# Performance work log

Measured on AMD Instinct MI355X. Metric: run time of the kernel, lower is better.

## Reference

```python
import jax, jax.numpy as jnp
import numpy as np

N = 100000   # nodes
E = 1600000  # edges
F = 256      # n_feats
H = 128      # n_hidden
HEADS = 8
C = 64       # n_class


def setup_inputs() -> dict:
    key = jax.random.key(0)
    ks = jax.random.split(key, 32)
    rn = lambda k, shape, s=0.05: jax.random.normal(k, shape, jnp.float32) * s
    return {
        'x': rn(ks[0], (N, F), 1.0),
        'src': jax.random.randint(ks[1], (E,), 0, N, jnp.int32),
        'dst': jax.random.randint(ks[2], (E,), 0, N, jnp.int32),
        'in_W': rn(ks[3], (F, H)), 'in_b': jnp.zeros((H,), jnp.float32),
        # layer 0 (concat=True, dim_out = H // HEADS)
        'q0_W': rn(ks[4], (H, H)), 'q0_b': jnp.zeros((H,), jnp.float32),
        'k0_W': rn(ks[5], (H, H)), 'k0_b': jnp.zeros((H,), jnp.float32),
        'v0_W': rn(ks[6], (H, H)), 'v0_b': jnp.zeros((H,), jnp.float32),
        'res0_W': rn(ks[7], (H, H)), 'res0_b': jnp.zeros((H,), jnp.float32),
        'gate0_W': rn(ks[8], (3 * H, 1)),
        'ln0_g': jnp.ones((H,), jnp.float32), 'ln0_b': jnp.zeros((H,), jnp.float32),
        # layer 1 (last: dim_out = C per head, concat=False, only_gate residual)
        'q1_W': rn(ks[9], (H, C * HEADS)), 'q1_b': jnp.zeros((C * HEADS,), jnp.float32),
        'k1_W': rn(ks[10], (H, C * HEADS)), 'k1_b': jnp.zeros((C * HEADS,), jnp.float32),
        'v1_W': rn(ks[11], (H, C * HEADS)), 'v1_b': jnp.zeros((C * HEADS,), jnp.float32),
        'res1_W': rn(ks[12], (H, C)), 'res1_b': jnp.zeros((C,), jnp.float32),
        'gate1_W': rn(ks[13], (3 * C, 1)),
    }


def _attn(x, qW, qb, kW, kb, vW, vb, src, dst, concat):
    n = x.shape[0]
    q = (x @ qW + qb).reshape(n, HEADS, -1)
    k = (x @ kW + kb).reshape(n, HEADS, -1)
    v = (x @ vW + vb).reshape(n, HEADS, -1)
    d = q.shape[-1]
    # u_dot_v: per-edge dot(q[src], k[dst]) -> [E, HEADS]
    s = jnp.einsum('ehd,ehd->eh', q[src], k[dst]) / jnp.sqrt(jnp.float32(d))
    # edge_softmax: segment softmax over incoming edges of each dst node
    m = jax.ops.segment_max(s, dst, num_segments=n)
    e = jnp.exp(s - m[dst])
    z = jax.ops.segment_sum(e, dst, num_segments=n)
    p = e / z[dst]
    # u_mul_e_sum: scatter-add v[src] * p to dst
    out = jax.ops.segment_sum(v[src] * p[:, :, None], dst, num_segments=n)
    return out.reshape(n, -1) if concat else out.mean(axis=1)


def _layernorm(x, g, b, eps=1e-5):
    mu = x.mean(-1, keepdims=True)
    var = ((x - mu) ** 2).mean(-1, keepdims=True)
    return (x - mu) / jnp.sqrt(var + eps) * g + b


def _gated_res(x, res, rW, rb, gW, ln_g=None, ln_b=None, only_gate=False):
    res = res @ rW + rb
    gate = jax.nn.sigmoid(jnp.concatenate([x, res, x - res], axis=-1) @ gW)
    out = x * gate + res * (1.0 - gate)
    if only_gate:
        return out
    return jax.nn.relu(_layernorm(out, ln_g, ln_b))


def reference(x, src, dst, in_W, in_b,
              q0_W, q0_b, k0_W, k0_b, v0_W, v0_b, res0_W, res0_b, gate0_W, ln0_g, ln0_b,
              q1_W, q1_b, k1_W, k1_b, v1_W, v1_b, res1_W, res1_b, gate1_W):
    h = x @ in_W + in_b
    a0 = _attn(h, q0_W, q0_b, k0_W, k0_b, v0_W, v0_b, src, dst, concat=True)
    h = _gated_res(a0, h, res0_W, res0_b, gate0_W, ln0_g, ln0_b, only_gate=False)
    a1 = _attn(h, q1_W, q1_b, k1_W, k1_b, v1_W, v1_b, src, dst, concat=False)
    out = _gated_res(a1, h, res1_W, res1_b, gate1_W, only_gate=True)
    return out
```

## Files before the change

kernel.cpp:

```cpp
#include <hip/hip_runtime.h>


typedef unsigned short u16;
typedef __attribute__((ext_vector_type(8))) unsigned short ushort8;
typedef __attribute__((ext_vector_type(8))) short short8v;
typedef __attribute__((ext_vector_type(4))) float f32x4;
typedef __attribute__((ext_vector_type(2))) float f32x2;

__device__ __forceinline__ float bf2f(unsigned short u) {
    return __uint_as_float(((unsigned)u) << 16);
}
__device__ __forceinline__ unsigned short f2bf(float f) {
    unsigned u = __float_as_uint(f);
    unsigned r = 0x7fffu + ((u >> 16) & 1u);
    return (unsigned short)((u + r) >> 16);
}
__device__ __forceinline__ unsigned char f2fp8(float f) {
    return (unsigned char)__builtin_amdgcn_cvt_pk_fp8_f32(f, 0.f, 0, false);
}

__device__ __forceinline__ void gload16(const void* gp, const void* lp) {
    __builtin_amdgcn_global_load_lds(
        (const __attribute__((address_space(1))) unsigned*)(uintptr_t)gp,
        (__attribute__((address_space(3))) unsigned*)(unsigned)(uintptr_t)lp,
        16, 0, 0);
}

__global__ void prep_k(const float* __restrict__ q1W, const float* __restrict__ k1W,
                       const float* __restrict__ v1W, const float* __restrict__ r1W,
                       u16* __restrict__ arena) {
    int i = blockIdx.x * 256 + threadIdx.x + 98304;
    if (i >= 303104) return;
    float val;
    if (i < 294912) {
        int j = i - 98304;
        int row = j >> 7, kk = j & 127;
        int p = row / 768, rr = row - p * 768;
        int sec = rr >> 8, c = p * 256 + (rr & 255);
        const float* s = (sec == 0) ? q1W : (sec == 1) ? k1W : v1W;
        val = s[kk * 512 + c];
    } else {
        int j = i - 294912;
        int n = j >> 7, kk = j & 127;
        val = r1W[kk * 64 + n];
    }
    arena[i] = f2bf(val);
}

__global__ void cw_k(const float* __restrict__ inW, const float* __restrict__ in_b,
                     const float* __restrict__ q0W, const float* __restrict__ k0W,
                     const float* __restrict__ v0W, const float* __restrict__ r0W,
                     const float* __restrict__ q0b, const float* __restrict__ k0b,
                     const float* __restrict__ v0b, const float* __restrict__ r0b,
                     u16* __restrict__ cwt, float* __restrict__ cwb) {
    int i = blockIdx.x * 256 + threadIdx.x;
    if (i < 131072) {
        int n = i >> 8, k = i & 255;
        int sec = n >> 7, c = n & 127;
        const float* s = (sec == 0) ? q0W : (sec == 1) ? k0W : (sec == 2) ? v0W : r0W;
        float acc = 0.f;
        for (int j = 0; j < 128; ++j) acc = fmaf(inW[k * 128 + j], s[j * 128 + c], acc);
        cwt[(size_t)n * 256 + k] = f2bf(acc);
    } else if (i < 131584) {
        int n = i - 131072;
        int sec = n >> 7, c = n & 127;
        const float* s = (sec == 0) ? q0W : (sec == 1) ? k0W : (sec == 2) ? v0W : r0W;
        const float* b = (sec == 0) ? q0b : (sec == 1) ? k0b : (sec == 2) ? v0b : r0b;
        float acc = b[c];
        for (int j = 0; j < 128; ++j) acc = fmaf(in_b[j], s[j * 128 + c], acc);
        cwb[n] = acc;
    }
}

__global__ void bias_k(const float* __restrict__ q1b, const float* __restrict__ k1b,
                       const float* __restrict__ v1b, const float* __restrict__ r1b,
                       float* __restrict__ out) {
    int i = blockIdx.x * 256 + threadIdx.x;
    if (i >= 1600) return;
    if (i < 1536) {
        int p = i / 768, rr = i - p * 768;
        int sec = rr >> 8, c = p * 256 + (rr & 255);
        out[i] = (sec == 0) ? q1b[c] : (sec == 1) ? k1b[c] : v1b[c];
    } else {
        out[i] = r1b[i - 1536];
    }
}

__global__ void cvt_k(const float* __restrict__ in, u16* __restrict__ out, int n8) {
    int i = blockIdx.x * 256 + threadIdx.x;
    if (i >= n8) return;
    float4 a = *(const float4*)(in + (size_t)i * 8);
    float4 b = *(const float4*)(in + (size_t)i * 8 + 4);
    ushort8 o = {f2bf(a.x), f2bf(a.y), f2bf(a.z), f2bf(a.w),
                 f2bf(b.x), f2bf(b.y), f2bf(b.z), f2bf(b.w)};
    *(ushort8*)(out + (size_t)i * 8) = o;
}

template <int MODE, int K>
__global__ __launch_bounds__(256) void mgemm7(const u16* __restrict__ A,
                                              const u16* __restrict__ Bt,
                                              const float* __restrict__ bias,
                                              void* __restrict__ C,
                                              float* __restrict__ C2,
                                              int M, int MB, int ny, int Nvalid) {
    __shared__ __align__(16) unsigned char smem[36864];
    u16* As = (u16*)smem;
    u16* Bs = (u16*)(smem + 16384);
    int id = blockIdx.x;
    int xcd = id & 7, rest = id >> 3;
    int y = rest % ny;
    int x = (rest / ny) * 8 + xcd;
    if (x >= MB) return;
    const int bm = x * 128;
    const int bn = y * 128;
    const int t = threadIdx.x, lane = t & 63, wid = t >> 6;
    const int wm = (wid >> 1) * 64, wn = (wid & 1) * 64;
    const int jlog = ((lane & 7) ^ (lane >> 3)) * 8;
    f32x4 acc[4][4] = {};
    for (int k0 = 0; k0 < K; k0 += 64) {
#pragma unroll
        for (int c2 = 0; c2 < 4; ++c2) {
            int seg = c2 * 4 + wid;
            int row = seg * 8 + (lane >> 3);
            int ga = bm + row; if (ga >= M) ga = 0;
            gload16(A + (size_t)ga * K + k0 + jlog, (const char*)As + seg * 1024);
            int gb = bn + row; if (gb >= Nvalid) gb = 0;
            gload16(Bt + (size_t)gb * K + k0 + jlog, (const char*)Bs + seg * 1024);
        }
        __syncthreads();
#pragma unroll
        for (int ks = 0; ks < 2; ++ks) {
            const int jx = ks * 4 + (lane >> 4);
            short8v af[4], bfr[4];
#pragma unroll
            for (int i = 0; i < 4; ++i) {
                int ra = wm + i * 16 + (lane & 15);
                af[i] = *(const short8v*)((const char*)As + ra * 128 + ((jx ^ (ra & 7)) << 4));
                int rb = wn + i * 16 + (lane & 15);
                bfr[i] = *(const short8v*)((const char*)Bs + rb * 128 + ((jx ^ (rb & 7)) << 4));
            }
#pragma unroll
            for (int mi = 0; mi < 4; ++mi)
#pragma unroll
                for (int ni = 0; ni < 4; ++ni)
                    acc[mi][ni] = __builtin_amdgcn_mfma_f32_16x16x32_bf16(
                        af[mi], bfr[ni], acc[mi][ni], 0, 0, 0);
        }
        if (k0 + 64 < K) __syncthreads();
    }
    const int sec = y;
    bool fp8lds = false;
    int gsecoff = 0, rowbytes = 0;
    if (MODE == 1) {
        if (sec == 0)      { fp8lds = true; gsecoff = 0;   rowbytes = 512; }
        else if (sec == 2) { fp8lds = true; gsecoff = 384; rowbytes = 512; }
    } else if (MODE >= 2) {
        if (sec < 2)                  { fp8lds = true; gsecoff = sec * 128;             rowbytes = 1024; }
        else if (sec >= 4 && sec < 6) { fp8lds = true; gsecoff = 768 + (sec - 4) * 128; rowbytes = 1024; }
    }
    if (fp8lds) {
        unsigned char* tile = smem;
        __syncthreads();
#pragma unroll
        for (int ni = 0; ni < 4; ++ni) {
            int lcol = wn + ni * 16 + (lane & 15);
            float bs = bias[bn + lcol];
#pragma unroll
            for (int mi = 0; mi < 4; ++mi) {
#pragma unroll
                for (int j = 0; j < 4; ++j) {
                    int lrow = wm + mi * 16 + (lane >> 4) * 4 + j;
                    float val = acc[mi][ni][j] + bs;
                    tile[lrow * 144 + ((((lcol >> 4) ^ (lrow & 7)) << 4) | (lcol & 15))] =
                        f2fp8(val * 16.f);
                }
            }
        }
        __syncthreads();
#pragma unroll
        for (int it = 0; it < 4; ++it) {
            int lin = it * 256 + t;
            int row = lin >> 3, ch = lin & 7;
            int crow = bm + row;
            if (crow < M) {
                const float4 vsrc = *(const float4*)(tile + row * 144 + ((ch ^ (row & 7)) << 4));
                *(float4*)((unsigned char*)C + (size_t)crow * rowbytes + gsecoff + ch * 16) = vsrc;
            }
        }
        return;
    }
    bool bf16lds = false;
    if (MODE == 1 && sec == 1)             { bf16lds = true; gsecoff = 128; rowbytes = 512; }
    else if (MODE >= 2 && sec >= 2 && sec < 4) {
        bf16lds = true; gsecoff = 256 + (sec - 2) * 256; rowbytes = 1024;
    }
    if (bf16lds) {
        unsigned char* tile = smem;
        __syncthreads();
#pragma unroll
        for (int ni = 0; ni < 4; ++ni) {
            int lcol = wn + ni * 16 + (lane & 15);
            float bs = bias[bn + lcol];
            int by = lcol * 2, ch = by >> 4;
#pragma unroll
            for (int mi = 0; mi < 4; ++mi) {
#pragma unroll
                for (int j = 0; j < 4; ++j) {
                    int lrow = wm + mi * 16 + (lane >> 4) * 4 + j;
                    float val = acc[mi][ni][j] + bs;
                    *(u16*)(tile + lrow * 272 + ((ch ^ (lrow & 7)) << 4) + (by & 15)) = f2bf(val);
                }
            }
        }
        __syncthreads();
#pragma unroll
        for (int it = 0; it < 8; ++it) {
            int lin = it * 256 + t;
            int row = lin >> 4, ch = lin & 15;
            int crow = bm + row;
            if (crow < M) {
                const float4 vsrc = *(const float4*)(tile + row * 272 + ((ch ^ (row & 7)) << 4));
                *(float4*)((unsigned char*)C + (size_t)crow * rowbytes + gsecoff + ch * 16) = vsrc;
            }
        }
        return;
    }
#pragma unroll
    for (int ni = 0; ni < 4; ++ni) {
        int lcol = wn + ni * 16 + (lane & 15);
        int ccol = bn + lcol;
        if (ccol >= Nvalid) continue;
        float bs = bias[ccol];
#pragma unroll
        for (int mi = 0; mi < 4; ++mi) {
#pragma unroll
            for (int j = 0; j < 4; ++j) {
                int crow = bm + wm + mi * 16 + (lane >> 4) * 4 + j;
                if (crow >= M) continue;
                float val = acc[mi][ni][j] + bs;
                if (MODE == 1) {
                    C2[(size_t)crow * 128 + lcol] = val;
                } else {
                    C2[(size_t)crow * 64 + lcol] = val;
                }
            }
        }
    }
}

__global__ void zero1_k(int* __restrict__ a, int n) {
    int i = blockIdx.x * 256 + threadIdx.x;
    if (i < n) a[i] = 0;
}

__global__ void hist_k(const int* __restrict__ dst, int* __restrict__ cnt,
                       int* __restrict__ rank, int E) {
    int i = blockIdx.x * 256 + threadIdx.x;
    if (i < E) rank[i] = atomicAdd(&cnt[dst[i]], 1);
}

__global__ void blocksum_k(const int* __restrict__ cnt, int* __restrict__ bsum, int n) {
    __shared__ int sd[256];
    int i = blockIdx.x * 256 + threadIdx.x;
    sd[threadIdx.x] = (i < n) ? cnt[i] : 0;
    __syncthreads();
    for (int off = 128; off > 0; off >>= 1) {
        if (threadIdx.x < off) sd[threadIdx.x] += sd[threadIdx.x + off];
        __syncthreads();
    }
    if (threadIdx.x == 0) bsum[blockIdx.x] = sd[0];
}

__global__ void scanb_k(int* bsum, int nb) {
    __shared__ int tmp[512];
    int t = threadIdx.x;
    tmp[t] = (t < nb) ? bsum[t] : 0;
    __syncthreads();
    for (int off = 1; off < 512; off <<= 1) {
        int v = (t >= off) ? tmp[t - off] : 0;
        __syncthreads();
        tmp[t] += v;
        __syncthreads();
    }
    if (t < nb) bsum[t] = (t ? tmp[t - 1] : 0);
}

__global__ void scanc_k(const int* __restrict__ cnt, const int* __restrict__ bsum,
                        int* __restrict__ row_off, int n, int E) {
    __shared__ int tmp[256];
    int b = blockIdx.x, t = threadIdx.x;
    int i = b * 256 + t;
    int own = (i < n) ? cnt[i] : 0;
    tmp[t] = own;
    __syncthreads();
    for (int off = 1; off < 256; off <<= 1) {
        int v = (t >= off) ? tmp[t - off] : 0;
        __syncthreads();
        tmp[t] += v;
        __syncthreads();
    }
    if (i < n) row_off[i] = bsum[b] + tmp[t] - own;
    if (b == 0 && t == 0) row_off[n] = E;
}

__global__ void scatter_k(const int* __restrict__ src, const int* __restrict__ dst,
                          const int* __restrict__ row_off, const int* __restrict__ rank,
                          int* __restrict__ csr_src, int E) {
    int i = blockIdx.x * 256 + threadIdx.x;
    if (i < E) csr_src[row_off[dst[i]] + rank[i]] = src[i];
}

__global__ __launch_bounds__(256) void attn0_k(const unsigned char* __restrict__ qkv,
                                               const int* __restrict__ row_off,
                                               const int* __restrict__ csr,
                                               const float* __restrict__ res0o,
                                               const float* __restrict__ gw,
                                               const float* __restrict__ lng,
                                               const float* __restrict__ lnb,
                                               u16* __restrict__ h1, int n) {
    int w = (blockIdx.x * 256 + threadIdx.x) >> 6;
    int lane = threadIdx.x & 63;
    if (w >= n) return;
    int beg = row_off[w], end = row_off[w + 1];
    unsigned kv = *(const unsigned*)(qkv + (size_t)w * 512 + 128 + 4 * lane);
    const float KS = (0.25f / 16.f) * 1.44269504f;
    float k0f = bf2f((u16)kv) * KS, k1f = bf2f((u16)(kv >> 16)) * KS;
    float den = 0.f, num0 = 0.f, num1 = 0.f;
    int e = beg;
    for (; e + 4 <= end; e += 4) {
        int s0 = csr[e], s1 = csr[e + 1], s2 = csr[e + 2], s3 = csr[e + 3];
        const unsigned char* r0 = qkv + (size_t)s0 * 512;
        const unsigned char* r1 = qkv + (size_t)s1 * 512;
        const unsigned char* r2 = qkv + (size_t)s2 * 512;
        const unsigned char* r3 = qkv + (size_t)s3 * 512;
        int qa = *(const unsigned short*)(r0 + 2 * lane);
        int qb = *(const unsigned short*)(r1 + 2 * lane);
        int qc = *(const unsigned short*)(r2 + 2 * lane);
        int qd = *(const unsigned short*)(r3 + 2 * lane);
        int va = *(const unsigned short*)(r0 + 384 + 2 * lane);
        int vb = *(const unsigned short*)(r1 + 384 + 2 * lane);
        int vc = *(const unsigned short*)(r2 + 384 + 2 * lane);
        int vd = *(const unsigned short*)(r3 + 384 + 2 * lane);
        f32x2 qaf = __builtin_amdgcn_cvt_pk_f32_fp8(qa, false);
        f32x2 qbf = __builtin_amdgcn_cvt_pk_f32_fp8(qb, false);
        f32x2 qcf = __builtin_amdgcn_cvt_pk_f32_fp8(qc, false);
        f32x2 qdf = __builtin_amdgcn_cvt_pk_f32_fp8(qd, false);
        float pa = qaf.x * k0f + qaf.y * k1f;
        float pb = qbf.x * k0f + qbf.y * k1f;
        float pc = qcf.x * k0f + qcf.y * k1f;
        float pd = qdf.x * k0f + qdf.y * k1f;
#pragma unroll
        for (int off = 1; off < 8; off <<= 1) {
            pa += __shfl_xor(pa, off); pb += __shfl_xor(pb, off);
            pc += __shfl_xor(pc, off); pd += __shfl_xor(pd, off);
        }
        float wa = exp2f(pa), wb = exp2f(pb);
        float wc = exp2f(pc), wd = exp2f(pd);
        den += (wa + wb) + (wc + wd);
        f32x2 vaf = __builtin_amdgcn_cvt_pk_f32_fp8(va, false);
        f32x2 vbf = __builtin_amdgcn_cvt_pk_f32_fp8(vb, false);
        f32x2 vcf = __builtin_amdgcn_cvt_pk_f32_fp8(vc, false);
        f32x2 vdf = __builtin_amdgcn_cvt_pk_f32_fp8(vd, false);
        num0 = fmaf(wa, vaf.x, num0); num1 = fmaf(wa, vaf.y, num1);
        num0 = fmaf(wb, vbf.x, num0); num1 = fmaf(wb, vbf.y, num1);
        num0 = fmaf(wc, vcf.x, num0); num1 = fmaf(wc, vcf.y, num1);
        num0 = fmaf(wd, vdf.x, num0); num1 = fmaf(wd, vdf.y, num1);
    }
    for (; e < end; ++e) {
        int s = csr[e];
        const unsigned char* r = qkv + (size_t)s * 512;
        int qv = *(const unsigned short*)(r + 2 * lane);
        f32x2 qf = __builtin_amdgcn_cvt_pk_f32_fp8(qv, false);
        float p = qf.x * k0f + qf.y * k1f;
        p += __shfl_xor(p, 1);
        p += __shfl_xor(p, 2);
        p += __shfl_xor(p, 4);
        float wt = exp2f(p);
        den += wt;
        int vv = *(const unsigned short*)(r + 384 + 2 * lane);
        f32x2 vf = __builtin_amdgcn_cvt_pk_f32_fp8(vv, false);
        num0 = fmaf(wt, vf.x, num0); num1 = fmaf(wt, vf.y, num1);
    }
    float inv = (end > beg) ? (1.f / den) * (1.f / 16.f) : 0.f;
    float x1 = num0 * inv, x2 = num1 * inv;
    f32x2 rv  = *(const f32x2*)(res0o + (size_t)w * 128 + 2 * lane);
    f32x2 ga  = *(const f32x2*)(gw + 2 * lane);
    f32x2 gb  = *(const f32x2*)(gw + 128 + 2 * lane);
    f32x2 gc  = *(const f32x2*)(gw + 256 + 2 * lane);
    float ca1 = ga.x + gc.x, ca2 = ga.y + gc.y;
    float cr1 = gb.x - gc.x, cr2 = gb.y - gc.y;
    float dot = x1 * ca1 + x2 * ca2 + rv.x * cr1 + rv.y * cr2;
#pragma unroll
    for (int off = 1; off < 64; off <<= 1) dot += __shfl_xor(dot, off);
    float g = 1.f / (1.f + __expf(-dot));
    float o1 = x1 * g + rv.x * (1.f - g);
    float o2 = x2 * g + rv.y * (1.f - g);
    float s = o1 + o2;
#pragma unroll
    for (int off = 1; off < 64; off <<= 1) s += __shfl_xor(s, off);
    float mu = s * (1.f / 128.f);
    float d1 = o1 - mu, d2 = o2 - mu;
    float vs = d1 * d1 + d2 * d2;
#pragma unroll
    for (int off = 1; off < 64; off <<= 1) vs += __shfl_xor(vs, off);
    float rstd = rsqrtf(vs * (1.f / 128.f) + 1e-5f);
    f32x2 lg = *(const f32x2*)(lng + 2 * lane);
    f32x2 lb = *(const f32x2*)(lnb + 2 * lane);
    float y1 = fmaxf(d1 * rstd * lg.x + lb.x, 0.f);
    float y2 = fmaxf(d2 * rstd * lg.y + lb.y, 0.f);
    unsigned pk = (unsigned)f2bf(y1) | ((unsigned)f2bf(y2) << 16);
    ((unsigned*)h1)[(size_t)w * 64 + lane] = pk;
}

__device__ __forceinline__ void attn1_core(const unsigned char* __restrict__ qkv,
                                           const int* __restrict__ csr,
                                           int w, int lane, int beg, int end,
                                           float& o0, float& o1, float& o2, float& o3) {
    const float KS = (0.125f / 16.f) * 1.44269504f;
    float kr0, kr1, kr2, kr3;
    {
        uint2 kk2 = *(const uint2*)(qkv + (size_t)w * 1024 + 256 + 8 * lane);
        kr0 = bf2f((u16)kk2.x) * KS; kr1 = bf2f((u16)(kk2.x >> 16)) * KS;
        kr2 = bf2f((u16)kk2.y) * KS; kr3 = bf2f((u16)(kk2.y >> 16)) * KS;
    }
    float den = 0.f, num0 = 0.f, num1 = 0.f, num2 = 0.f, num3 = 0.f;
    int e = beg;
    for (; e + 4 <= end; e += 4) {
        int s0 = csr[e], s1 = csr[e + 1], s2 = csr[e + 2], s3 = csr[e + 3];
        const unsigned char* r0 = qkv + (size_t)s0 * 1024;
        const unsigned char* r1 = qkv + (size_t)s1 * 1024;
        const unsigned char* r2 = qkv + (size_t)s2 * 1024;
        const unsigned char* r3 = qkv + (size_t)s3 * 1024;
        unsigned qa = *(const unsigned*)(r0 + 4 * lane);
        unsigned qb = *(const unsigned*)(r1 + 4 * lane);
        unsigned qc = *(const unsigned*)(r2 + 4 * lane);
        unsigned qd = *(const unsigned*)(r3 + 4 * lane);
        unsigned va = *(const unsigned*)(r0 + 768 + 4 * lane);
        unsigned vb = *(const unsigned*)(r1 + 768 + 4 * lane);
        unsigned vc = *(const unsigned*)(r2 + 768 + 4 * lane);
        unsigned vd = *(const unsigned*)(r3 + 768 + 4 * lane);
        f32x2 qa0 = __builtin_amdgcn_cvt_pk_f32_fp8((int)qa, false);
        f32x2 qa1 = __builtin_amdgcn_cvt_pk_f32_fp8((int)qa, true);
        f32x2 qb0 = __builtin_amdgcn_cvt_pk_f32_fp8((int)qb, false);
        f32x2 qb1 = __builtin_amdgcn_cvt_pk_f32_fp8((int)qb, true);
        f32x2 qc0 = __builtin_amdgcn_cvt_pk_f32_fp8((int)qc, false);
        f32x2 qc1 = __builtin_amdgcn_cvt_pk_f32_fp8((int)qc, true);
        f32x2 qd0 = __builtin_amdgcn_cvt_pk_f32_fp8((int)qd, false);
        f32x2 qd1 = __builtin_amdgcn_cvt_pk_f32_fp8((int)qd, true);
        float pa = qa0.x * kr0 + qa0.y * kr1 + qa1.x * kr2 + qa1.y * kr3;
        float pb = qb0.x * kr0 + qb0.y * kr1 + qb1.x * kr2 + qb1.y * kr3;
        float pc = qc0.x * kr0 + qc0.y * kr1 + qc1.x * kr2 + qc1.y * kr3;
        float pd = qd0.x * kr0 + qd0.y * kr1 + qd1.x * kr2 + qd1.y * kr3;
#pragma unroll
        for (int off = 1; off < 16; off <<= 1) {
            pa += __shfl_xor(pa, off); pb += __shfl_xor(pb, off);
            pc += __shfl_xor(pc, off); pd += __shfl_xor(pd, off);
        }
        float wa = exp2f(pa), wb = exp2f(pb);
        float wc = exp2f(pc), wd = exp2f(pd);
        den += (wa + wb) + (wc + wd);
        f32x2 va0 = __builtin_amdgcn_cvt_pk_f32_fp8((int)va, false);
        f32x2 va1 = __builtin_amdgcn_cvt_pk_f32_fp8((int)va, true);
        f32x2 vb0 = __builtin_amdgcn_cvt_pk_f32_fp8((int)vb, false);
        f32x2 vb1 = __builtin_amdgcn_cvt_pk_f32_fp8((int)vb, true);
        f32x2 vc0 = __builtin_amdgcn_cvt_pk_f32_fp8((int)vc, false);
        f32x2 vc1 = __builtin_amdgcn_cvt_pk_f32_fp8((int)vc, true);
        f32x2 vd0 = __builtin_amdgcn_cvt_pk_f32_fp8((int)vd, false);
        f32x2 vd1 = __builtin_amdgcn_cvt_pk_f32_fp8((int)vd, true);
        num0 = fmaf(wa, va0.x, num0); num1 = fmaf(wa, va0.y, num1);
        num2 = fmaf(wa, va1.x, num2); num3 = fmaf(wa, va1.y, num3);
        num0 = fmaf(wb, vb0.x, num0); num1 = fmaf(wb, vb0.y, num1);
        num2 = fmaf(wb, vb1.x, num2); num3 = fmaf(wb, vb1.y, num3);
        num0 = fmaf(wc, vc0.x, num0); num1 = fmaf(wc, vc0.y, num1);
        num2 = fmaf(wc, vc1.x, num2); num3 = fmaf(wc, vc1.y, num3);
        num0 = fmaf(wd, vd0.x, num0); num1 = fmaf(wd, vd0.y, num1);
        num2 = fmaf(wd, vd1.x, num2); num3 = fmaf(wd, vd1.y, num3);
    }
    for (; e < end; ++e) {
        int s = csr[e];
        const unsigned char* r = qkv + (size_t)s * 1024;
        unsigned qv = *(const unsigned*)(r + 4 * lane);
        f32x2 q0 = __builtin_amdgcn_cvt_pk_f32_fp8((int)qv, false);
        f32x2 q1 = __builtin_amdgcn_cvt_pk_f32_fp8((int)qv, true);
        float p = q0.x * kr0 + q0.y * kr1 + q1.x * kr2 + q1.y * kr3;
#pragma unroll
        for (int off = 1; off < 16; off <<= 1) p += __shfl_xor(p, off);
        float wt = exp2f(p);
        den += wt;
        unsigned vv = *(const unsigned*)(r + 768 + 4 * lane);
        f32x2 v0 = __builtin_amdgcn_cvt_pk_f32_fp8((int)vv, false);
        f32x2 v1 = __builtin_amdgcn_cvt_pk_f32_fp8((int)vv, true);
        num0 = fmaf(wt, v0.x, num0); num1 = fmaf(wt, v0.y, num1);
        num2 = fmaf(wt, v1.x, num2); num3 = fmaf(wt, v1.y, num3);
    }
    float inv = (end > beg) ? 1.f / den : 0.f;
    o0 = num0 * inv; o1 = num1 * inv; o2 = num2 * inv; o3 = num3 * inv;
    o0 += __shfl_xor(o0, 16); o1 += __shfl_xor(o1, 16);
    o2 += __shfl_xor(o2, 16); o3 += __shfl_xor(o3, 16);
    o0 += __shfl_xor(o0, 32); o1 += __shfl_xor(o1, 32);
    o2 += __shfl_xor(o2, 32); o3 += __shfl_xor(o3, 32);
}

__global__ __launch_bounds__(256) void attn1f_k(const unsigned char* __restrict__ qkv,
                                                const int* __restrict__ row_off,
                                                const int* __restrict__ csr,
                                                float* __restrict__ out, int n) {
    int w = (blockIdx.x * 256 + threadIdx.x) >> 6;
    int lane = threadIdx.x & 63;
    if (w >= n) return;
    int beg = row_off[w], end = row_off[w + 1];
    float o0, o1, o2, o3;
    attn1_core(qkv, csr, w, lane, beg, end, o0, o1, o2, o3);
    if (lane < 16) {
        const float HS = 1.f / 128.f;
        *(float4*)(out + ((size_t)w << 6) + lane * 4) =
            make_float4(o0 * HS, o1 * HS, o2 * HS, o3 * HS);
    }
}

__global__ __launch_bounds__(256) void attn1g_k(const unsigned char* __restrict__ qkv,
                                                const int* __restrict__ row_off,
                                                const int* __restrict__ csr,
                                                const float* __restrict__ a1,
                                                const float* __restrict__ res1o,
                                                const float* __restrict__ gw,
                                                float* __restrict__ out, int n) {
    int w = (blockIdx.x * 256 + threadIdx.x) >> 6;
    int lane = threadIdx.x & 63;
    if (w >= n) return;
    int beg = row_off[w], end = row_off[w + 1];
    float o0, o1, o2, o3;
    attn1_core(qkv, csr, w, lane, beg, end, o0, o1, o2, o3);
    const float HS = 1.f / 128.f;
    int ll = lane & 15;
    size_t base = (size_t)w * 64 + ll * 4;
    float4 ap = *(const float4*)(a1 + base);
    float4 rp = *(const float4*)(res1o + base);
    float4 g0 = *(const float4*)(gw + ll * 4);
    float4 g1 = *(const float4*)(gw + 64 + ll * 4);
    float4 g2 = *(const float4*)(gw + 128 + ll * 4);
    float xv0 = ap.x + o0 * HS, xv1 = ap.y + o1 * HS;
    float xv2 = ap.z + o2 * HS, xv3 = ap.w + o3 * HS;
    float dot = xv0 * (g0.x + g2.x) + xv1 * (g0.y + g2.y)
              + xv2 * (g0.z + g2.z) + xv3 * (g0.w + g2.w)
              + rp.x * (g1.x - g2.x) + rp.y * (g1.y - g2.y)
              + rp.z * (g1.z - g2.z) + rp.w * (g1.w - g2.w);
#pragma unroll
    for (int off = 1; off < 16; off <<= 1) dot += __shfl_xor(dot, off);
    float g = 1.f / (1.f + __expf(-dot));
    if (lane < 16) {
        float4 ov;
        ov.x = xv0 * g + rp.x * (1.f - g);
        ov.y = xv1 * g + rp.y * (1.f - g);
        ov.z = xv2 * g + rp.z * (1.f - g);
        ov.w = xv3 * g + rp.w * (1.f - g);
        *(float4*)(out + base) = ov;
    }
}

extern "C" void kernel_launch(void* const* d_in, const int* in_sizes, int n_in,
                              void* d_out, int out_size, void* d_ws, size_t ws_size,
                              hipStream_t stream) {
    const float* x    = (const float*)d_in[0];
    const int*   src  = (const int*)d_in[1];
    const int*   dst  = (const int*)d_in[2];
    const float* in_W = (const float*)d_in[3];
    const float* in_b = (const float*)d_in[4];
    const float* q0W = (const float*)d_in[5];  const float* q0b = (const float*)d_in[6];
    const float* k0W = (const float*)d_in[7];  const float* k0b = (const float*)d_in[8];
    const float* v0W = (const float*)d_in[9];  const float* v0b = (const float*)d_in[10];
    const float* r0W = (const float*)d_in[11]; const float* r0b = (const float*)d_in[12];
    const float* g0W = (const float*)d_in[13];
    const float* ln0g = (const float*)d_in[14]; const float* ln0b = (const float*)d_in[15];
    const float* q1W = (const float*)d_in[16]; const float* q1b = (const float*)d_in[17];
    const float* k1W = (const float*)d_in[18]; const float* k1b = (const float*)d_in[19];
    const float* v1W = (const float*)d_in[20]; const float* v1b = (const float*)d_in[21];
    const float* r1W = (const float*)d_in[22]; const float* r1b = (const float*)d_in[23];
    const float* g1W = (const float*)d_in[24];

    const int N = in_sizes[0] / 256;
    const int E = in_sizes[1];
    (void)ws_size; (void)n_in; (void)out_size;

    auto rnd = [](size_t b) { return (b + 255) & ~(size_t)255; };
    char* base = (char*)d_ws;
    const size_t S_f = rnd((size_t)N * 128 * 4);
    size_t o = 0;
    int* row_off = (int*)(base + o); o += rnd(((size_t)N + 1) * 4);
    int* csr     = (int*)(base + o); o += rnd((size_t)E * 4);
    u16* warena  = (u16*)(base + o); o += rnd((size_t)(303104 + 131072) * 2);
    float* barena = (float*)(base + o); o += rnd((size_t)(1600 + 512) * 4);
    char* RB = base + o;
    int* cnt  = (int*)RB;
    int* bsum = (int*)(RB + rnd((size_t)N * 4));
    unsigned char* QKV0 = (unsigned char*)RB;
    unsigned char* PASS = (unsigned char*)RB;
    float* res0o = (float*)(RB + S_f);
    u16*   x_bf  = (u16*)(RB + 2 * S_f);
    float* a1    = (float*)(RB + 2 * S_f);
    float* res1o = (float*)(RB + 2 * S_f + rnd((size_t)N * 64 * 4));
    int*   rank  = (int*)(RB + 3 * S_f);
    u16*   h1    = (u16*)(RB + 3 * S_f);

    u16* qkv1t0 = warena + 98304;
    u16* qkv1t1 = warena + 196608;
    u16* cwt    = warena + 303104;
    float* qkv1b = barena;
    float* cwb   = barena + 1600;

    dim3 blk(256);
    int nwb = (N * 64 + 255) / 256;
    int nb  = (N + 255) / 256;
    int mb  = (N + 127) / 128;
    int xch = (mb + 7) / 8;

    prep_k<<<(303104 - 98304 + 255) / 256, blk, 0, stream>>>(q1W, k1W, v1W, r1W, warena);
    cw_k<<<(131584 + 255) / 256, blk, 0, stream>>>(in_W, in_b, q0W, k0W, v0W, r0W,
                                                   q0b, k0b, v0b, r0b, cwt, cwb);
    bias_k<<<7, blk, 0, stream>>>(q1b, k1b, v1b, r1b, barena);
    cvt_k<<<(N * 32 + 255) / 256, blk, 0, stream>>>(x, x_bf, N * 32);

    zero1_k<<<nb, blk, 0, stream>>>(cnt, N);
    hist_k<<<(E + 255) / 256, blk, 0, stream>>>(dst, cnt, rank, E);
    blocksum_k<<<nb, blk, 0, stream>>>(cnt, bsum, N);
    scanb_k<<<1, 512, 0, stream>>>(bsum, nb);
    scanc_k<<<nb, blk, 0, stream>>>(cnt, bsum, row_off, N, E);
    scatter_k<<<(E + 255) / 256, blk, 0, stream>>>(src, dst, row_off, rank, csr, E);

    mgemm7<1, 256><<<8 * 4 * xch, blk, 0, stream>>>(x_bf, cwt, cwb, QKV0, res0o,
                                                    N, mb, 4, 512);
    attn0_k<<<nwb, blk, 0, stream>>>(QKV0, row_off, csr, res0o, g0W, ln0g, ln0b, h1, N);

    mgemm7<2, 128><<<8 * 6 * xch, blk, 0, stream>>>(h1, qkv1t0, qkv1b, PASS,
                                                    nullptr, N, mb, 6, 768);
    attn1f_k<<<nwb, blk, 0, stream>>>(PASS, row_off, csr, a1, N);

    mgemm7<3, 128><<<8 * 7 * xch, blk, 0, stream>>>(h1, qkv1t1, qkv1b + 768, PASS,
                                                    res1o, N, mb, 7, 832);
    attn1g_k<<<nwb, blk, 0, stream>>>(PASS, row_off, csr, a1, res1o, g1W,
                                      (float*)d_out, N);
}
```

Before: 730.7 us.

## Fuse layer-1 split GEMMs and attention passes into one GEMM plus one attention

Layer 1 used to run as two halves, each with its own GEMM and attention pass, with K stored in bf16 and an intermediate a1 buffer. Now a single GEMM produces Q, K and V for all heads in fp8 with a 1536-byte row stride, and writes the residual projection straight into the output buffer. One attention kernel then processes 8 lanes per head group with 8 elements per lane and applies the gate in the same pass. This removes a launch pair, one CSR traversal and the a1/res1o round trips, at the cost of storing K in fp8 (lower precision) and higher register use per lane.

```diff
diff --git a/kernel.cpp b/kernel.cpp
--- a/kernel.cpp
+++ b/kernel.cpp
@@ -29,21 +29,14 @@
 __global__ void prep_k(const float* __restrict__ q1W, const float* __restrict__ k1W,
                        const float* __restrict__ v1W, const float* __restrict__ r1W,
                        u16* __restrict__ arena) {
-    int i = blockIdx.x * 256 + threadIdx.x + 98304;
-    if (i >= 303104) return;
+    int i = blockIdx.x * 256 + threadIdx.x;
+    if (i >= 204800) return;
+    int row = i >> 7, kk = i & 127;
     float val;
-    if (i < 294912) {
-        int j = i - 98304;
-        int row = j >> 7, kk = j & 127;
-        int p = row / 768, rr = row - p * 768;
-        int sec = rr >> 8, c = p * 256 + (rr & 255);
-        const float* s = (sec == 0) ? q1W : (sec == 1) ? k1W : v1W;
-        val = s[kk * 512 + c];
-    } else {
-        int j = i - 294912;
-        int n = j >> 7, kk = j & 127;
-        val = r1W[kk * 64 + n];
-    }
+    if (row < 512)       val = q1W[kk * 512 + row];
+    else if (row < 1024) val = k1W[kk * 512 + row - 512];
+    else if (row < 1536) val = v1W[kk * 512 + row - 1024];
+    else                 val = r1W[kk * 64 + (row - 1536)];
     arena[i] = f2bf(val);
 }
 
@@ -77,13 +70,10 @@
                        float* __restrict__ out) {
     int i = blockIdx.x * 256 + threadIdx.x;
     if (i >= 1600) return;
-    if (i < 1536) {
-        int p = i / 768, rr = i - p * 768;
-        int sec = rr >> 8, c = p * 256 + (rr & 255);
-        out[i] = (sec == 0) ? q1b[c] : (sec == 1) ? k1b[c] : v1b[c];
-    } else {
-        out[i] = r1b[i - 1536];
-    }
+    if (i < 512)       out[i] = q1b[i];
+    else if (i < 1024) out[i] = k1b[i - 512];
+    else if (i < 1536) out[i] = v1b[i - 1024];
+    else               out[i] = r1b[i - 1536];
 }
 
 __global__ void cvt_k(const float* __restrict__ in, u16* __restrict__ out, int n8) {
@@ -154,9 +144,8 @@
     if (MODE == 1) {
         if (sec == 0)      { fp8lds = true; gsecoff = 0;   rowbytes = 512; }
         else if (sec == 2) { fp8lds = true; gsecoff = 384; rowbytes = 512; }
-    } else if (MODE >= 2) {
-        if (sec < 2)                  { fp8lds = true; gsecoff = sec * 128;             rowbytes = 1024; }
-        else if (sec >= 4 && sec < 6) { fp8lds = true; gsecoff = 768 + (sec - 4) * 128; rowbytes = 1024; }
+    } else {
+        if (sec < 12)      { fp8lds = true; gsecoff = sec * 128; rowbytes = 1536; }
     }
     if (fp8lds) {
         unsigned char* tile = smem;
@@ -189,12 +178,7 @@
         }
         return;
     }
-    bool bf16lds = false;
-    if (MODE == 1 && sec == 1)             { bf16lds = true; gsecoff = 128; rowbytes = 512; }
-    else if (MODE >= 2 && sec >= 2 && sec < 4) {
-        bf16lds = true; gsecoff = 256 + (sec - 2) * 256; rowbytes = 1024;
-    }
-    if (bf16lds) {
+    if (MODE == 1 && sec == 1) {
         unsigned char* tile = smem;
         __syncthreads();
 #pragma unroll
@@ -220,7 +204,7 @@
             int crow = bm + row;
             if (crow < M) {
                 const float4 vsrc = *(const float4*)(tile + row * 272 + ((ch ^ (row & 7)) << 4));
-                *(float4*)((unsigned char*)C + (size_t)crow * rowbytes + gsecoff + ch * 16) = vsrc;
+                *(float4*)((unsigned char*)C + (size_t)crow * 512 + 128 + ch * 16) = vsrc;
             }
         }
         return;
@@ -238,11 +222,8 @@
                 int crow = bm + wm + mi * 16 + (lane >> 4) * 4 + j;
                 if (crow >= M) continue;
                 float val = acc[mi][ni][j] + bs;
-                if (MODE == 1) {
-                    C2[(size_t)crow * 128 + lcol] = val;
-                } else {
-                    C2[(size_t)crow * 64 + lcol] = val;
-                }
+                if (MODE == 1) C2[(size_t)crow * 128 + lcol] = val;
+                else           C2[(size_t)crow * 64 + lcol] = val;
             }
         }
     }
@@ -412,149 +393,139 @@
     ((unsigned*)h1)[(size_t)w * 64 + lane] = pk;
 }
 
-__device__ __forceinline__ void attn1_core(const unsigned char* __restrict__ qkv,
-                                           const int* __restrict__ csr,
-                                           int w, int lane, int beg, int end,
-                                           float& o0, float& o1, float& o2, float& o3) {
-    const float KS = (0.125f / 16.f) * 1.44269504f;
-    float kr0, kr1, kr2, kr3;
-    {
-        uint2 kk2 = *(const uint2*)(qkv + (size_t)w * 1024 + 256 + 8 * lane);
-        kr0 = bf2f((u16)kk2.x) * KS; kr1 = bf2f((u16)(kk2.x >> 16)) * KS;
-        kr2 = bf2f((u16)kk2.y) * KS; kr3 = bf2f((u16)(kk2.y >> 16)) * KS;
-    }
-    float den = 0.f, num0 = 0.f, num1 = 0.f, num2 = 0.f, num3 = 0.f;
-    int e = beg;
-    for (; e + 4 <= end; e += 4) {
-        int s0 = csr[e], s1 = csr[e + 1], s2 = csr[e + 2], s3 = csr[e + 3];
-        const unsigned char* r0 = qkv + (size_t)s0 * 1024;
-        const unsigned char* r1 = qkv + (size_t)s1 * 1024;
-        const unsigned char* r2 = qkv + (size_t)s2 * 1024;
-        const unsigned char* r3 = qkv + (size_t)s3 * 1024;
-        unsigned qa = *(const unsigned*)(r0 + 4 * lane);
-        unsigned qb = *(const unsigned*)(r1 + 4 * lane);
-        unsigned qc = *(const unsigned*)(r2 + 4 * lane);
-        unsigned qd = *(const unsigned*)(r3 + 4 * lane);
-        unsigned va = *(const unsigned*)(r0 + 768 + 4 * lane);
-        unsigned vb = *(const unsigned*)(r1 + 768 + 4 * lane);
-        unsigned vc = *(const unsigned*)(r2 + 768 + 4 * lane);
-        unsigned vd = *(const unsigned*)(r3 + 768 + 4 * lane);
-        f32x2 qa0 = __builtin_amdgcn_cvt_pk_f32_fp8((int)qa, false);
-        f32x2 qa1 = __builtin_amdgcn_cvt_pk_f32_fp8((int)qa, true);
-        f32x2 qb0 = __builtin_amdgcn_cvt_pk_f32_fp8((int)qb, false);
-        f32x2 qb1 = __builtin_amdgcn_cvt_pk_f32_fp8((int)qb, true);
-        f32x2 qc0 = __builtin_amdgcn_cvt_pk_f32_fp8((int)qc, false);
-        f32x2 qc1 = __builtin_amdgcn_cvt_pk_f32_fp8((int)qc, true);
-        f32x2 qd0 = __builtin_amdgcn_cvt_pk_f32_fp8((int)qd, false);
-        f32x2 qd1 = __builtin_amdgcn_cvt_pk_f32_fp8((int)qd, true);
-        float pa = qa0.x * kr0 + qa0.y * kr1 + qa1.x * kr2 + qa1.y * kr3;
-        float pb = qb0.x * kr0 + qb0.y * kr1 + qb1.x * kr2 + qb1.y * kr3;
-        float pc = qc0.x * kr0 + qc0.y * kr1 + qc1.x * kr2 + qc1.y * kr3;
-        float pd = qd0.x * kr0 + qd0.y * kr1 + qd1.x * kr2 + qd1.y * kr3;
-#pragma unroll
-        for (int off = 1; off < 16; off <<= 1) {
-            pa += __shfl_xor(pa, off); pb += __shfl_xor(pb, off);
-            pc += __shfl_xor(pc, off); pd += __shfl_xor(pd, off);
-        }
-        float wa = exp2f(pa), wb = exp2f(pb);
-        float wc = exp2f(pc), wd = exp2f(pd);
-        den += (wa + wb) + (wc + wd);
-        f32x2 va0 = __builtin_amdgcn_cvt_pk_f32_fp8((int)va, false);
-        f32x2 va1 = __builtin_amdgcn_cvt_pk_f32_fp8((int)va, true);
-        f32x2 vb0 = __builtin_amdgcn_cvt_pk_f32_fp8((int)vb, false);
-        f32x2 vb1 = __builtin_amdgcn_cvt_pk_f32_fp8((int)vb, true);
-        f32x2 vc0 = __builtin_amdgcn_cvt_pk_f32_fp8((int)vc, false);
-        f32x2 vc1 = __builtin_amdgcn_cvt_pk_f32_fp8((int)vc, true);
-        f32x2 vd0 = __builtin_amdgcn_cvt_pk_f32_fp8((int)vd, false);
-        f32x2 vd1 = __builtin_amdgcn_cvt_pk_f32_fp8((int)vd, true);
-        num0 = fmaf(wa, va0.x, num0); num1 = fmaf(wa, va0.y, num1);
-        num2 = fmaf(wa, va1.x, num2); num3 = fmaf(wa, va1.y, num3);
-        num0 = fmaf(wb, vb0.x, num0); num1 = fmaf(wb, vb0.y, num1);
-        num2 = fmaf(wb, vb1.x, num2); num3 = fmaf(wb, vb1.y, num3);
-        num0 = fmaf(wc, vc0.x, num0); num1 = fmaf(wc, vc0.y, num1);
-        num2 = fmaf(wc, vc1.x, num2); num3 = fmaf(wc, vc1.y, num3);
-        num0 = fmaf(wd, vd0.x, num0); num1 = fmaf(wd, vd0.y, num1);
-        num2 = fmaf(wd, vd1.x, num2); num3 = fmaf(wd, vd1.y, num3);
-    }
-    for (; e < end; ++e) {
-        int s = csr[e];
-        const unsigned char* r = qkv + (size_t)s * 1024;
-        unsigned qv = *(const unsigned*)(r + 4 * lane);
-        f32x2 q0 = __builtin_amdgcn_cvt_pk_f32_fp8((int)qv, false);
-        f32x2 q1 = __builtin_amdgcn_cvt_pk_f32_fp8((int)qv, true);
-        float p = q0.x * kr0 + q0.y * kr1 + q1.x * kr2 + q1.y * kr3;
-#pragma unroll
-        for (int off = 1; off < 16; off <<= 1) p += __shfl_xor(p, off);
-        float wt = exp2f(p);
-        den += wt;
-        unsigned vv = *(const unsigned*)(r + 768 + 4 * lane);
-        f32x2 v0 = __builtin_amdgcn_cvt_pk_f32_fp8((int)vv, false);
-        f32x2 v1 = __builtin_amdgcn_cvt_pk_f32_fp8((int)vv, true);
-        num0 = fmaf(wt, v0.x, num0); num1 = fmaf(wt, v0.y, num1);
-        num2 = fmaf(wt, v1.x, num2); num3 = fmaf(wt, v1.y, num3);
-    }
-    float inv = (end > beg) ? 1.f / den : 0.f;
-    o0 = num0 * inv; o1 = num1 * inv; o2 = num2 * inv; o3 = num3 * inv;
-    o0 += __shfl_xor(o0, 16); o1 += __shfl_xor(o1, 16);
-    o2 += __shfl_xor(o2, 16); o3 += __shfl_xor(o3, 16);
-    o0 += __shfl_xor(o0, 32); o1 += __shfl_xor(o1, 32);
-    o2 += __shfl_xor(o2, 32); o3 += __shfl_xor(o3, 32);
-}
-
-__global__ __launch_bounds__(256) void attn1f_k(const unsigned char* __restrict__ qkv,
+__global__ __launch_bounds__(256) void attn1s_k(const unsigned char* __restrict__ qkv,
                                                 const int* __restrict__ row_off,
                                                 const int* __restrict__ csr,
-                                                float* __restrict__ out, int n) {
-    int w = (blockIdx.x * 256 + threadIdx.x) >> 6;
-    int lane = threadIdx.x & 63;
-    if (w >= n) return;
-    int beg = row_off[w], end = row_off[w + 1];
-    float o0, o1, o2, o3;
-    attn1_core(qkv, csr, w, lane, beg, end, o0, o1, o2, o3);
-    if (lane < 16) {
-        const float HS = 1.f / 128.f;
-        *(float4*)(out + ((size_t)w << 6) + lane * 4) =
-            make_float4(o0 * HS, o1 * HS, o2 * HS, o3 * HS);
-    }
-}
-
-__global__ __launch_bounds__(256) void attn1g_k(const unsigned char* __restrict__ qkv,
-                                                const int* __restrict__ row_off,
-                                                const int* __restrict__ csr,
-                                                const float* __restrict__ a1,
-                                                const float* __restrict__ res1o,
                                                 const float* __restrict__ gw,
                                                 float* __restrict__ out, int n) {
     int w = (blockIdx.x * 256 + threadIdx.x) >> 6;
     int lane = threadIdx.x & 63;
     if (w >= n) return;
     int beg = row_off[w], end = row_off[w + 1];
-    float o0, o1, o2, o3;
-    attn1_core(qkv, csr, w, lane, beg, end, o0, o1, o2, o3);
+    const float KS = 1.44269504f / 2048.f;
+    float kr[8];
+    {
+        uint2 kk = *(const uint2*)(qkv + (size_t)w * 1536 + 512 + 8 * lane);
+        f32x2 k0 = __builtin_amdgcn_cvt_pk_f32_fp8((int)kk.x, false);
+        f32x2 k1 = __builtin_amdgcn_cvt_pk_f32_fp8((int)kk.x, true);
+        f32x2 k2 = __builtin_amdgcn_cvt_pk_f32_fp8((int)kk.y, false);
+        f32x2 k3 = __builtin_amdgcn_cvt_pk_f32_fp8((int)kk.y, true);
+        kr[0] = k0.x * KS; kr[1] = k0.y * KS; kr[2] = k1.x * KS; kr[3] = k1.y * KS;
+        kr[4] = k2.x * KS; kr[5] = k2.y * KS; kr[6] = k3.x * KS; kr[7] = k3.y * KS;
+    }
+    float den = 0.f;
+    float num[8] = {};
+    int e = beg;
+    for (; e + 2 <= end; e += 2) {
+        int s0 = csr[e], s1 = csr[e + 1];
+        const unsigned char* r0 = qkv + (size_t)s0 * 1536;
+        const unsigned char* r1 = qkv + (size_t)s1 * 1536;
+        uint2 qa = *(const uint2*)(r0 + 8 * lane);
+        uint2 qb = *(const uint2*)(r1 + 8 * lane);
+        uint2 va = *(const uint2*)(r0 + 1024 + 8 * lane);
+        uint2 vb = *(const uint2*)(r1 + 1024 + 8 * lane);
+        f32x2 a0 = __builtin_amdgcn_cvt_pk_f32_fp8((int)qa.x, false);
+        f32x2 a1 = __builtin_amdgcn_cvt_pk_f32_fp8((int)qa.x, true);
+        f32x2 a2 = __builtin_amdgcn_cvt_pk_f32_fp8((int)qa.y, false);
+        f32x2 a3 = __builtin_amdgcn_cvt_pk_f32_fp8((int)qa.y, true);
+        f32x2 b0 = __builtin_amdgcn_cvt_pk_f32_fp8((int)qb.x, false);
+        f32x2 b1 = __builtin_amdgcn_cvt_pk_f32_fp8((int)qb.x, true);
+        f32x2 b2 = __builtin_amdgcn_cvt_pk_f32_fp8((int)qb.y, false);
+        f32x2 b3 = __builtin_amdgcn_cvt_pk_f32_fp8((int)qb.y, true);
+        float pa = a0.x * kr[0] + a0.y * kr[1] + a1.x * kr[2] + a1.y * kr[3]
+                 + a2.x * kr[4] + a2.y * kr[5] + a3.x * kr[6] + a3.y * kr[7];
+        float pb = b0.x * kr[0] + b0.y * kr[1] + b1.x * kr[2] + b1.y * kr[3]
+                 + b2.x * kr[4] + b2.y * kr[5] + b3.x * kr[6] + b3.y * kr[7];
+        pa += __shfl_xor(pa, 1); pb += __shfl_xor(pb, 1);
+        pa += __shfl_xor(pa, 2); pb += __shfl_xor(pb, 2);
+        pa += __shfl_xor(pa, 4); pb += __shfl_xor(pb, 4);
+        float wa = exp2f(pa), wb = exp2f(pb);
+        den += wa + wb;
+        f32x2 c0 = __builtin_amdgcn_cvt_pk_f32_fp8((int)va.x, false);
+        f32x2 c1 = __builtin_amdgcn_cvt_pk_f32_fp8((int)va.x, true);
+        f32x2 c2 = __builtin_amdgcn_cvt_pk_f32_fp8((int)va.y, false);
+        f32x2 c3 = __builtin_amdgcn_cvt_pk_f32_fp8((int)va.y, true);
+        f32x2 d0 = __builtin_amdgcn_cvt_pk_f32_fp8((int)vb.x, false);
+        f32x2 d1 = __builtin_amdgcn_cvt_pk_f32_fp8((int)vb.x, true);
+        f32x2 d2 = __builtin_amdgcn_cvt_pk_f32_fp8((int)vb.y, false);
+        f32x2 d3 = __builtin_amdgcn_cvt_pk_f32_fp8((int)vb.y, true);
+        num[0] = fmaf(wa, c0.x, num[0]); num[1] = fmaf(wa, c0.y, num[1]);
+        num[2] = fmaf(wa, c1.x, num[2]); num[3] = fmaf(wa, c1.y, num[3]);
+        num[4] = fmaf(wa, c2.x, num[4]); num[5] = fmaf(wa, c2.y, num[5]);
+        num[6] = fmaf(wa, c3.x, num[6]); num[7] = fmaf(wa, c3.y, num[7]);
+        num[0] = fmaf(wb, d0.x, num[0]); num[1] = fmaf(wb, d0.y, num[1]);
+        num[2] = fmaf(wb, d1.x, num[2]); num[3] = fmaf(wb, d1.y, num[3]);
+        num[4] = fmaf(wb, d2.x, num[4]); num[5] = fmaf(wb, d2.y, num[5]);
+        num[6] = fmaf(wb, d3.x, num[6]); num[7] = fmaf(wb, d3.y, num[7]);
+    }
+    for (; e < end; ++e) {
+        int s = csr[e];
+        const unsigned char* r = qkv + (size_t)s * 1536;
+        uint2 qv = *(const uint2*)(r + 8 * lane);
+        f32x2 a0 = __builtin_amdgcn_cvt_pk_f32_fp8((int)qv.x, false);
+        f32x2 a1 = __builtin_amdgcn_cvt_pk_f32_fp8((int)qv.x, true);
+        f32x2 a2 = __builtin_amdgcn_cvt_pk_f32_fp8((int)qv.y, false);
+        f32x2 a3 = __builtin_amdgcn_cvt_pk_f32_fp8((int)qv.y, true);
+        float p = a0.x * kr[0] + a0.y * kr[1] + a1.x * kr[2] + a1.y * kr[3]
+                + a2.x * kr[4] + a2.y * kr[5] + a3.x * kr[6] + a3.y * kr[7];
+        p += __shfl_xor(p, 1);
+        p += __shfl_xor(p, 2);
+        p += __shfl_xor(p, 4);
+        float wt = exp2f(p);
+        den += wt;
+        uint2 vv = *(const uint2*)(r + 1024 + 8 * lane);
+        f32x2 c0 = __builtin_amdgcn_cvt_pk_f32_fp8((int)vv.x, false);
+        f32x2 c1 = __builtin_amdgcn_cvt_pk_f32_fp8((int)vv.x, true);
+        f32x2 c2 = __builtin_amdgcn_cvt_pk_f32_fp8((int)vv.y, false);
+        f32x2 c3 = __builtin_amdgcn_cvt_pk_f32_fp8((int)vv.y, true);
+        num[0] = fmaf(wt, c0.x, num[0]); num[1] = fmaf(wt, c0.y, num[1]);
+        num[2] = fmaf(wt, c1.x, num[2]); num[3] = fmaf(wt, c1.y, num[3]);
+        num[4] = fmaf(wt, c2.x, num[4]); num[5] = fmaf(wt, c2.y, num[5]);
+        num[6] = fmaf(wt, c3.x, num[6]); num[7] = fmaf(wt, c3.y, num[7]);
+    }
     const float HS = 1.f / 128.f;
-    int ll = lane & 15;
-    size_t base = (size_t)w * 64 + ll * 4;
-    float4 ap = *(const float4*)(a1 + base);
-    float4 rp = *(const float4*)(res1o + base);
-    float4 g0 = *(const float4*)(gw + ll * 4);
-    float4 g1 = *(const float4*)(gw + 64 + ll * 4);
-    float4 g2 = *(const float4*)(gw + 128 + ll * 4);
-    float xv0 = ap.x + o0 * HS, xv1 = ap.y + o1 * HS;
-    float xv2 = ap.z + o2 * HS, xv3 = ap.w + o3 * HS;
-    float dot = xv0 * (g0.x + g2.x) + xv1 * (g0.y + g2.y)
-              + xv2 * (g0.z + g2.z) + xv3 * (g0.w + g2.w)
-              + rp.x * (g1.x - g2.x) + rp.y * (g1.y - g2.y)
-              + rp.z * (g1.z - g2.z) + rp.w * (g1.w - g2.w);
-#pragma unroll
-    for (int off = 1; off < 16; off <<= 1) dot += __shfl_xor(dot, off);
+    float inv = (end > beg) ? (1.f / den) * HS : 0.f;
+    float o[8];
+#pragma unroll
+    for (int j = 0; j < 8; ++j) o[j] = num[j] * inv;
+#pragma unroll
+    for (int off = 8; off < 64; off <<= 1)
+#pragma unroll
+        for (int j = 0; j < 8; ++j) o[j] += __shfl_xor(o[j], off);
+    int ll = lane & 7;
+    size_t base = (size_t)w * 64 + ll * 8;
+    float4 rp0 = *(const float4*)(out + base);
+    float4 rp1 = *(const float4*)(out + base + 4);
+    float4 ga0 = *(const float4*)(gw + ll * 8);
+    float4 ga1 = *(const float4*)(gw + ll * 8 + 4);
+    float4 gb0 = *(const float4*)(gw + 64 + ll * 8);
+    float4 gb1 = *(const float4*)(gw + 64 + ll * 8 + 4);
+    float4 gc0 = *(const float4*)(gw + 128 + ll * 8);
+    float4 gc1 = *(const float4*)(gw + 128 + ll * 8 + 4);
+    float dot = o[0] * (ga0.x + gc0.x) + o[1] * (ga0.y + gc0.y)
+              + o[2] * (ga0.z + gc0.z) + o[3] * (ga0.w + gc0.w)
+              + o[4] * (ga1.x + gc1.x) + o[5] * (ga1.y + gc1.y)
+              + o[6] * (ga1.z + gc1.z) + o[7] * (ga1.w + gc1.w)
+              + rp0.x * (gb0.x - gc0.x) + rp0.y * (gb0.y - gc0.y)
+              + rp0.z * (gb0.z - gc0.z) + rp0.w * (gb0.w - gc0.w)
+              + rp1.x * (gb1.x - gc1.x) + rp1.y * (gb1.y - gc1.y)
+              + rp1.z * (gb1.z - gc1.z) + rp1.w * (gb1.w - gc1.w);
+    dot += __shfl_xor(dot, 1);
+    dot += __shfl_xor(dot, 2);
+    dot += __shfl_xor(dot, 4);
     float g = 1.f / (1.f + __expf(-dot));
-    if (lane < 16) {
-        float4 ov;
-        ov.x = xv0 * g + rp.x * (1.f - g);
-        ov.y = xv1 * g + rp.y * (1.f - g);
-        ov.z = xv2 * g + rp.z * (1.f - g);
-        ov.w = xv3 * g + rp.w * (1.f - g);
-        *(float4*)(out + base) = ov;
+    if (lane < 8) {
+        float4 ov0, ov1;
+        ov0.x = o[0] * g + rp0.x * (1.f - g);
+        ov0.y = o[1] * g + rp0.y * (1.f - g);
+        ov0.z = o[2] * g + rp0.z * (1.f - g);
+        ov0.w = o[3] * g + rp0.w * (1.f - g);
+        ov1.x = o[4] * g + rp1.x * (1.f - g);
+        ov1.y = o[5] * g + rp1.y * (1.f - g);
+        ov1.z = o[6] * g + rp1.z * (1.f - g);
+        ov1.w = o[7] * g + rp1.w * (1.f - g);
+        *(float4*)(out + base) = ov0;
+        *(float4*)(out + base + 4) = ov1;
     }
 }
 
@@ -588,7 +559,7 @@
     size_t o = 0;
     int* row_off = (int*)(base + o); o += rnd(((size_t)N + 1) * 4);
     int* csr     = (int*)(base + o); o += rnd((size_t)E * 4);
-    u16* warena  = (u16*)(base + o); o += rnd((size_t)(303104 + 131072) * 2);
+    u16* warena  = (u16*)(base + o); o += rnd((size_t)(204800 + 131072) * 2);
     float* barena = (float*)(base + o); o += rnd((size_t)(1600 + 512) * 4);
     char* RB = base + o;
     int* cnt  = (int*)RB;
@@ -597,14 +568,11 @@
     unsigned char* PASS = (unsigned char*)RB;
     float* res0o = (float*)(RB + S_f);
     u16*   x_bf  = (u16*)(RB + 2 * S_f);
-    float* a1    = (float*)(RB + 2 * S_f);
-    float* res1o = (float*)(RB + 2 * S_f + rnd((size_t)N * 64 * 4));
     int*   rank  = (int*)(RB + 3 * S_f);
     u16*   h1    = (u16*)(RB + 3 * S_f);
 
-    u16* qkv1t0 = warena + 98304;
-    u16* qkv1t1 = warena + 196608;
-    u16* cwt    = warena + 303104;
+    u16* qkv1t = warena;
+    u16* cwt   = warena + 204800;
     float* qkv1b = barena;
     float* cwb   = barena + 1600;
 
@@ -614,7 +582,7 @@
     int mb  = (N + 127) / 128;
     int xch = (mb + 7) / 8;
 
-    prep_k<<<(303104 - 98304 + 255) / 256, blk, 0, stream>>>(q1W, k1W, v1W, r1W, warena);
+    prep_k<<<(204800 + 255) / 256, blk, 0, stream>>>(q1W, k1W, v1W, r1W, qkv1t);
     cw_k<<<(131584 + 255) / 256, blk, 0, stream>>>(in_W, in_b, q0W, k0W, v0W, r0W,
                                                    q0b, k0b, v0b, r0b, cwt, cwb);
     bias_k<<<7, blk, 0, stream>>>(q1b, k1b, v1b, r1b, barena);
@@ -631,12 +599,7 @@
                                                     N, mb, 4, 512);
     attn0_k<<<nwb, blk, 0, stream>>>(QKV0, row_off, csr, res0o, g0W, ln0g, ln0b, h1, N);
 
-    mgemm7<2, 128><<<8 * 6 * xch, blk, 0, stream>>>(h1, qkv1t0, qkv1b, PASS,
-                                                    nullptr, N, mb, 6, 768);
-    attn1f_k<<<nwb, blk, 0, stream>>>(PASS, row_off, csr, a1, N);
-
-    mgemm7<3, 128><<<8 * 7 * xch, blk, 0, stream>>>(h1, qkv1t1, qkv1b + 768, PASS,
-                                                    res1o, N, mb, 7, 832);
-    attn1g_k<<<nwb, blk, 0, stream>>>(PASS, row_off, csr, a1, res1o, g1W,
-                                      (float*)d_out, N);
-}
+    mgemm7<4, 128><<<8 * 13 * xch, blk, 0, stream>>>(h1, qkv1t, qkv1b, PASS,
+                                                     (float*)d_out, N, mb, 13, 1600);
+    attn1s_k<<<nwb, blk, 0, stream>>>(PASS, row_off, csr, g1W, (float*)d_out, N);
+}
```

Result: faster. 678.2 us (-7.2%).
